# Kernel tuning notes

Measured on AMD Instinct MI355X. Metric: run time of the kernel, lower is better.

The kernel has to match this reference:

```python
import jax, jax.numpy as jnp
import numpy as np

K = 4
V = 32000
H = 512
B = 16
SOS = 1
EOS = 2


def setup_inputs() -> dict:
    key = jax.random.key(0)
    ks = jax.random.split(key, 8)
    s = 0.08  # small init keeps GRU/log_softmax well-conditioned
    return {
        "enc_h": jax.random.normal(ks[0], (B, H), jnp.float32),
        "E": jax.random.normal(ks[1], (V, H), jnp.float32) * s,
        "W_ih": jax.random.normal(ks[2], (H, 3 * H), jnp.float32) * s,
        "W_hh": jax.random.normal(ks[3], (H, 3 * H), jnp.float32) * s,
        "b_ih": jax.random.normal(ks[4], (3 * H,), jnp.float32) * s,
        "b_hh": jax.random.normal(ks[5], (3 * H,), jnp.float32) * s,
        "Wo": jax.random.normal(ks[6], (H, V), jnp.float32) * s,
        "bo": jax.random.normal(ks[7], (V,), jnp.float32) * s,
        "max_length": 32,
    }


def _beam_search(enc_h, E, W_ih, W_hh, b_ih, b_hh, Wo, bo, T):
    BK = B * K
    pos = jnp.arange(B, dtype=jnp.int32) * K  # pos_index
    # torch .repeat beam inflation: tiled layout (index i -> original i % B)
    h0 = jnp.tile(enc_h, (K, 1))  # [BK, H]
    inp0 = jnp.full((BK,), SOS, dtype=jnp.int32)
    ss0 = jnp.full((BK,), -jnp.inf, dtype=enc_h.dtype).at[pos].set(0.0)

    def gru(x, h):
        gi = x @ W_ih + b_ih
        gh = h @ W_hh + b_hh
        ir, iz, inn = jnp.split(gi, 3, axis=-1)
        hr, hz, hn = jnp.split(gh, 3, axis=-1)
        r = jax.nn.sigmoid(ir + hr)
        z = jax.nn.sigmoid(iz + hz)
        n = jnp.tanh(inn + r * hn)
        return (1.0 - z) * n + z * h

    def fwd_step(carry, _):
        inp, h, ss = carry
        h_new = gru(E[inp], h)                                   # [BK, H]
        logp = jax.nn.log_softmax(h_new @ Wo + bo, axis=-1)      # [BK, V]
        total = (ss[:, None] + logp).reshape(B, K * V)
        scores, cand = jax.lax.top_k(total, K)                   # [B, K]
        symbols = (cand % V).astype(jnp.int32).reshape(-1)       # input_var
        preds = (cand // V + pos[:, None]).astype(jnp.int32).reshape(-1)
        h_sel = h_new[preds]                                     # index_select hidden
        ss_new = scores.reshape(-1)
        ss_masked = jnp.where(symbols == EOS, -jnp.inf, ss_new)  # EOS masking
        return (symbols, h_sel, ss_masked), (logp, ss_new, preds, symbols, h_sel)

    _, (logps, step_scores, preds, syms, hiddens) = jax.lax.scan(
        fwd_step, (inp0, h0, ss0), None, length=T)

    # ---------------- backtrack ----------------
    last = step_scores[-1].reshape(B, K)
    s0, sorted_idx = jax.lax.top_k(last, K)
    tpred0 = (sorted_idx.astype(jnp.int32) + pos[:, None]).reshape(-1)
    lens0 = jnp.full((B, K), T, dtype=jnp.int32)
    hn0 = jnp.zeros((BK, H), dtype=enc_h.dtype)
    eos0 = jnp.zeros((B,), dtype=jnp.int32)

    def bt_step(carry, xs):
        tpred, eosf, s, lens, hn = carry
        logp_t, hid_t, pred_t, sym_t, score_t, tt = xs
        cur_out = logp_t[tpred]
        cur_hid = hid_t[tpred]
        cur_sym = sym_t[tpred]
        new_pred = pred_t[tpred]
        eos = sym_t == EOS
        eos_bk = eos.reshape(B, K).astype(jnp.int32)
        # original loop processes eos hits in descending beam order per batch
        higher = jnp.cumsum(eos_bk[:, ::-1], axis=1)[:, ::-1] - eos_bk
        occ = eosf[:, None] + higher
        res_k = K - occ % K - 1
        res_flat = (pos[:, None] + res_k).reshape(-1)
        idx = jnp.where(eos, res_flat, BK)  # BK = out of bounds -> dropped
        new_pred = new_pred.at[idx].set(pred_t, mode='drop')
        cur_out = cur_out.at[idx].set(logp_t, mode='drop')
        cur_hid = cur_hid.at[idx].set(hid_t, mode='drop')
        hn = hn.at[idx].set(hid_t, mode='drop')
        cur_sym = cur_sym.at[idx].set(sym_t, mode='drop')
        s = s.reshape(-1).at[idx].set(score_t, mode='drop').reshape(B, K)
        lens = lens.reshape(-1).at[idx].set(tt + 1, mode='drop').reshape(B, K)
        eosf = eosf + eos_bk.sum(axis=1)
        return (new_pred, eosf, s, lens, hn), (cur_out, cur_sym)

    ts = jnp.arange(T - 1, -1, -1, dtype=jnp.int32)
    (_, _, s_fin, lens_fin, hn_fin), (outs_rev, syms_rev) = jax.lax.scan(
        bt_step, (tpred0, eos0, s0, lens0, hn0),
        (logps[::-1], hiddens[::-1], preds[::-1], syms[::-1], step_scores[::-1], ts))

    s_sorted, re_idx = jax.lax.top_k(s_fin, K)
    lens_sorted = jnp.take_along_axis(lens_fin, re_idx, axis=1)
    re_flat = (re_idx.astype(jnp.int32) + pos[:, None]).reshape(-1)
    outs = outs_rev[::-1][:, re_flat].reshape(T, B, K, V)
    seqs = syms_rev[::-1][:, re_flat].reshape(T, B, K)
    decoder_outputs = outs[:, :, 0, :]            # [T, B, V]
    decoder_hidden = hn_fin[re_flat].reshape(B, K, H)[:, 0, :]
    return decoder_outputs, decoder_hidden, s_sorted, lens_sorted, seqs


def reference(enc_h, E, W_ih, W_hh, b_ih, b_hh, Wo, bo, max_length):
    return _beam_search(enc_h, E, W_ih, W_hh, b_ih, b_hh, Wo, bo, int(max_length))
```

## Files before the change

kernel.cpp:

```cpp
#include <hip/hip_runtime.h>
#include <math.h>
#include <limits.h>

#define T_STEPS 32
#define BATCH   16
#define KBEAM   4
#define BKR     64
#define HD      512
#define VOC     32000
#define G3      1536
#define SOS_TOK 1
#define EOS_TOK 2
#define NSP     (VOC/64)
#define NE      (NSP*4)

#define OFF_HCUR   ((size_t)0)
#define OFF_GBUF   (OFF_HCUR + (size_t)BKR*HD)
#define OFF_HNEW   (OFF_GBUF + (size_t)2*BKR*G3)
#define OFF_LSE    (OFF_HNEW + (size_t)T_STEPS*BKR*HD)
#define OFF_SS     (OFF_LSE + (size_t)T_STEPS*BKR)
#define OFF_SCORES (OFF_SS + BKR)
#define OFF_HNFIN  (OFF_SCORES + (size_t)T_STEPS*BKR)
#define OFF_PV     (OFF_HNFIN + (size_t)BKR*HD)
#define OFF_PM     (OFF_PV + (size_t)BKR*NE)
#define OFF_PS     (OFF_PM + (size_t)BKR*NSP)
#define OFF_FEND   (OFF_PS + (size_t)BKR*NSP)
#define IOFF_INP    0
#define IOFF_PREDS  64
#define IOFF_SYMS   (IOFF_PREDS + T_STEPS*BKR)
#define IOFF_RMAP   (IOFF_SYMS + T_STEPS*BKR)
#define IOFF_PC     (IOFF_RMAP + T_STEPS*BATCH)
#define IOFF_END    (IOFF_PC + BKR*NE)

#define O_HID  ((size_t)T_STEPS*BATCH*VOC)
#define O_SSRT (O_HID + (size_t)BATCH*HD)
#define O_LENS (O_SSRT + BATCH*KBEAM)
#define O_SEQS (O_LENS + BATCH*KBEAM)

typedef short bf16x8 __attribute__((ext_vector_type(8)));
typedef float f32x4  __attribute__((ext_vector_type(4)));

__device__ __forceinline__ unsigned short f2bf(float x){
    unsigned u = __float_as_uint(x);
    return (unsigned short)((u + 0x7fffu + ((u >> 16) & 1u)) >> 16);
}
__device__ __forceinline__ float bf2f(unsigned short h){
    return __uint_as_float(((unsigned)h) << 16);
}

__device__ __forceinline__ void mfma_core(
    const float* __restrict__ Abase, const int* __restrict__ ridx, int mbase,
    const float* __restrict__ B, int ldb, int n0,
    unsigned short (&Ah)[64][40], unsigned short (&Al)[64][40],
    unsigned short (&Bh)[64][40], unsigned short (&Bl)[64][40],
    int (&sidx)[64], f32x4 (&acc)[4])
{
    const int tid = threadIdx.x;
    if (tid < 64) sidx[tid] = ridx ? ridx[mbase + tid] : (mbase + tid);
    #pragma unroll
    for (int g = 0; g < 4; ++g) acc[g] = (f32x4){0.f, 0.f, 0.f, 0.f};
    const int wave = tid >> 6, lane = tid & 63;
    const int am = tid >> 2, ak0 = (tid & 3) * 8;
    const int bn = tid & 63, br0 = (tid >> 6) * 8;
    __syncthreads();
    const float* bcol = B + n0 + bn;
    for (int kt = 0; kt < 16; ++kt){
        {
            const float* ap = Abase + (size_t)sidx[am] * HD + kt * 32 + ak0;
            float4 x0 = *(const float4*)ap, x1 = *(const float4*)(ap + 4);
            float xs[8] = {x0.x, x0.y, x0.z, x0.w, x1.x, x1.y, x1.z, x1.w};
            union { unsigned short u[8]; uint4 v; } h8, l8;
            #pragma unroll
            for (int j = 0; j < 8; ++j){
                unsigned short h = f2bf(xs[j]);
                h8.u[j] = h; l8.u[j] = f2bf(xs[j] - bf2f(h));
            }
            *(uint4*)&Ah[am][ak0] = h8.v;
            *(uint4*)&Al[am][ak0] = l8.v;
        }
        {
            const float* bp = bcol + (size_t)(kt * 32 + br0) * ldb;
            union { unsigned short u[8]; uint4 v; } h8, l8;
            #pragma unroll
            for (int j = 0; j < 8; ++j){
                float x = bp[(size_t)j * ldb];
                unsigned short h = f2bf(x);
                h8.u[j] = h; l8.u[j] = f2bf(x - bf2f(h));
            }
            *(uint4*)&Bh[bn][br0] = h8.v;
            *(uint4*)&Bl[bn][br0] = l8.v;
        }
        __syncthreads();
        bf16x8 bh = *(const bf16x8*)&Bh[wave * 16 + (lane & 15)][(lane >> 4) * 8];
        bf16x8 bl = *(const bf16x8*)&Bl[wave * 16 + (lane & 15)][(lane >> 4) * 8];
        #pragma unroll
        for (int g = 0; g < 4; ++g){
            bf16x8 ah = *(const bf16x8*)&Ah[g * 16 + (lane & 15)][(lane >> 4) * 8];
            bf16x8 al = *(const bf16x8*)&Al[g * 16 + (lane & 15)][(lane >> 4) * 8];
            acc[g] = __builtin_amdgcn_mfma_f32_16x16x32_bf16(ah, bh, acc[g], 0, 0, 0);
            acc[g] = __builtin_amdgcn_mfma_f32_16x16x32_bf16(ah, bl, acc[g], 0, 0, 0);
            acc[g] = __builtin_amdgcn_mfma_f32_16x16x32_bf16(al, bh, acc[g], 0, 0, 0);
        }
        __syncthreads();
    }
}

__device__ __forceinline__ void dump_C(f32x4 (&acc)[4], float (&Cs)[64][65], int wave, int lane){
    #pragma unroll
    for (int g = 0; g < 4; ++g){
        int row = g * 16 + (lane >> 4) * 4;
        int col = wave * 16 + (lane & 15);
        #pragma unroll
        for (int r = 0; r < 4; ++r) Cs[row + r][col] = acc[g][r];
    }
}

__global__ __launch_bounds__(256) void gates_mfma_kernel(
    const float* __restrict__ E, const int* __restrict__ inp, const float* __restrict__ h_cur,
    const float* __restrict__ W_ih, const float* __restrict__ W_hh,
    const float* __restrict__ b_ih, const float* __restrict__ b_hh,
    float* __restrict__ gbuf)
{
    __shared__ unsigned short Ah[64][40], Al[64][40], Bh[64][40], Bl[64][40];
    __shared__ int sidx[64];
    __shared__ float Cs[64][65];
    const int z = blockIdx.y;
    const int n0 = blockIdx.x * 64;
    const int tid = threadIdx.x;
    f32x4 acc[4];
    mfma_core(z ? h_cur : E, z ? nullptr : inp, 0,
              z ? W_hh : W_ih, G3, n0, Ah, Al, Bh, Bl, sidx, acc);
    dump_C(acc, Cs, tid >> 6, tid & 63);
    __syncthreads();
    const float* bias = z ? b_hh : b_ih;
    const int row = tid >> 2, c0 = (tid & 3) * 16;
    float* gp = gbuf + (size_t)z * BKR * G3 + (size_t)row * G3 + n0 + c0;
    #pragma unroll
    for (int q = 0; q < 4; ++q){
        float4 bz = *(const float4*)(bias + n0 + c0 + q * 4);
        float4 v;
        v.x = Cs[row][c0 + q*4 + 0] + bz.x;
        v.y = Cs[row][c0 + q*4 + 1] + bz.y;
        v.z = Cs[row][c0 + q*4 + 2] + bz.z;
        v.w = Cs[row][c0 + q*4 + 3] + bz.w;
        *(float4*)(gp + q * 4) = v;
    }
}

__global__ void gru_combine_kernel(const float* __restrict__ gbuf, const float* __restrict__ h_cur,
    float* __restrict__ h_new)
{
    int x = blockIdx.x * 256 + threadIdx.x;
    int i = x >> 9, j = x & 511;
    const float* gi = gbuf + (size_t)i * G3;
    const float* gh = gbuf + (size_t)BKR * G3 + (size_t)i * G3;
    float ir = gi[j], iz = gi[j + 512], inn = gi[j + 1024];
    float hr = gh[j], hz = gh[j + 512], hnv = gh[j + 1024];
    float r  = 1.f / (1.f + expf(-(ir + hr)));
    float zz = 1.f / (1.f + expf(-(iz + hz)));
    float n  = tanhf(inn + r * hnv);
    h_new[x] = (1.f - zz) * n + zz * h_cur[x];
}

__device__ __forceinline__ void ins4(float* bv, int* bc, float s, int c){
    bool g0 = (s > bv[0]) || (s == bv[0] && c < bc[0]);
    bool g1 = (s > bv[1]) || (s == bv[1] && c < bc[1]);
    bool g2 = (s > bv[2]) || (s == bv[2] && c < bc[2]);
    bool g3 = (s > bv[3]) || (s == bv[3] && c < bc[3]);
    if (g0){ bv[3]=bv[2];bc[3]=bc[2]; bv[2]=bv[1];bc[2]=bc[1]; bv[1]=bv[0];bc[1]=bc[0]; bv[0]=s; bc[0]=c; }
    else if (g1){ bv[3]=bv[2];bc[3]=bc[2]; bv[2]=bv[1];bc[2]=bc[1]; bv[1]=s; bc[1]=c; }
    else if (g2){ bv[3]=bv[2];bc[3]=bc[2]; bv[2]=s; bc[2]=c; }
    else if (g3){ bv[3]=s; bc[3]=c; }
}

__global__ __launch_bounds__(256) void logits_topk_kernel(const float* __restrict__ h_new,
    const float* __restrict__ Wo, const float* __restrict__ bo,
    float* __restrict__ pv, int* __restrict__ pc, float* __restrict__ pm, float* __restrict__ ps)
{
    __shared__ unsigned short Ah[64][40], Al[64][40], Bh[64][40], Bl[64][40];
    __shared__ int sidx[64];
    __shared__ float Cs[64][65];
    const int bx = blockIdx.x, n0 = bx * 64;
    const int tid = threadIdx.x;
    f32x4 acc[4];
    mfma_core(h_new, nullptr, 0, Wo, VOC, n0, Ah, Al, Bh, Bl, sidx, acc);
    dump_C(acc, Cs, tid >> 6, tid & 63);
    __syncthreads();
    const int row = tid >> 2, c0 = (tid & 3) * 16;
    float bv[4] = {-INFINITY,-INFINITY,-INFINITY,-INFINITY};
    int bc[4] = {INT_MAX, INT_MAX, INT_MAX, INT_MAX};
    float m = -INFINITY, s = 0.f;
    #pragma unroll
    for (int j = 0; j < 16; ++j){
        float x = Cs[row][c0 + j] + bo[n0 + c0 + j];
        if (x > m){ s = s * expf(m - x) + 1.f; m = x; }
        else s += expf(x - m);
        ins4(bv, bc, x, n0 + c0 + j);
    }
    #pragma unroll
    for (int o = 1; o < 4; o <<= 1){
        float ov[4]; int oc[4];
        #pragma unroll
        for (int q = 0; q < 4; ++q){ ov[q] = __shfl_xor(bv[q], o); oc[q] = __shfl_xor(bc[q], o); }
        #pragma unroll
        for (int q = 0; q < 4; ++q) ins4(bv, bc, ov[q], oc[q]);
        float m2 = __shfl_xor(m, o), s2 = __shfl_xor(s, o);
        float M = fmaxf(m, m2);
        s = s * expf(m - M) + s2 * expf(m2 - M);
        m = M;
    }
    if ((tid & 3) == 0){
        const size_t base = (size_t)row * NE + (size_t)bx * 4;
        #pragma unroll
        for (int q = 0; q < 4; ++q){ pv[base + q] = bv[q]; pc[base + q] = bc[q]; }
        pm[row * NSP + bx] = m; ps[row * NSP + bx] = s;
    }
}

__global__ __launch_bounds__(256) void final_mfma_kernel(const float* __restrict__ h_new_all,
    const int* __restrict__ rmap, const float* __restrict__ lse_all,
    const float* __restrict__ Wo, const float* __restrict__ bo, float* __restrict__ out)
{
    __shared__ unsigned short Ah[64][40], Al[64][40], Bh[64][40], Bl[64][40];
    __shared__ int sidx[64];
    __shared__ float Cs[64][65];
    __shared__ float subm[64];
    const int n0 = blockIdx.x * 64, mb = blockIdx.y * 64;
    const int tid = threadIdx.x;
    f32x4 acc[4];
    mfma_core(h_new_all, rmap, mb, Wo, VOC, n0, Ah, Al, Bh, Bl, sidx, acc);
    dump_C(acc, Cs, tid >> 6, tid & 63);
    if (tid < 64) subm[tid] = lse_all[sidx[tid]];
    __syncthreads();
    const int row = tid >> 2, c0 = (tid & 3) * 16;
    const float sub = subm[row];
    float* op = out + (size_t)(mb + row) * VOC + n0 + c0;
    #pragma unroll
    for (int q = 0; q < 4; ++q){
        float4 bz = *(const float4*)(bo + n0 + c0 + q * 4);
        float4 v;
        v.x = Cs[row][c0 + q*4 + 0] + bz.x - sub;
        v.y = Cs[row][c0 + q*4 + 1] + bz.y - sub;
        v.z = Cs[row][c0 + q*4 + 2] + bz.z - sub;
        v.w = Cs[row][c0 + q*4 + 3] + bz.w - sub;
        *(float4*)(op + q * 4) = v;
    }
}

__global__ __launch_bounds__(256) void topk_phase_b(
    const float* __restrict__ pv, const int* __restrict__ pc,
    const float* __restrict__ pm, const float* __restrict__ ps,
    int t,
    float* __restrict__ scores_all, int* __restrict__ preds_all, int* __restrict__ syms_all,
    float* __restrict__ ss, int* __restrict__ inp, float* __restrict__ lse_all,
    const float* __restrict__ h_new, float* __restrict__ h_cur)
{
    const int b = blockIdx.x, tid = threadIdx.x;
    const int wave = tid >> 6, lane = tid & 63;
    const int row = b * KBEAM + wave;

    float bv[4] = {-INFINITY,-INFINITY,-INFINITY,-INFINITY};
    int bc[4] = {INT_MAX, INT_MAX, INT_MAX, INT_MAX};
    for (int e = lane; e < NE; e += 64)
        ins4(bv, bc, pv[(size_t)row * NE + e], pc[(size_t)row * NE + e]);
    #pragma unroll
    for (int o = 1; o < 64; o <<= 1){
        float ov[4]; int oc[4];
        #pragma unroll
        for (int q = 0; q < 4; ++q){ ov[q] = __shfl_xor(bv[q], o); oc[q] = __shfl_xor(bc[q], o); }
        #pragma unroll
        for (int q = 0; q < 4; ++q) ins4(bv, bc, ov[q], oc[q]);
    }
    float m = -INFINITY, s = 0.f;
    for (int e = lane; e < NSP; e += 64){
        float m2 = pm[row * NSP + e], s2 = ps[row * NSP + e];
        float M = fmaxf(m, m2);
        s = s * expf(m - M) + s2 * expf(m2 - M);
        m = M;
    }
    #pragma unroll
    for (int o = 1; o < 64; o <<= 1){
        float m2 = __shfl_xor(m, o), s2 = __shfl_xor(s, o);
        float M = fmaxf(m, m2);
        s = s * expf(m - M) + s2 * expf(m2 - M);
        m = M;
    }
    __shared__ float rtv[KBEAM][4]; __shared__ int rtc[KBEAM][4];
    __shared__ float rlse[KBEAM];
    if (lane == 0){
        #pragma unroll
        for (int q = 0; q < 4; ++q){ rtv[wave][q] = bv[q]; rtc[wave][q] = bc[q]; }
        rlse[wave] = m + logf(s);
    }
    __syncthreads();
    __shared__ int spred[KBEAM];
    if (tid == 0){
        float gv[4] = {-INFINITY,-INFINITY,-INFINITY,-INFINITY};
        int gc[4] = {INT_MAX, INT_MAX, INT_MAX, INT_MAX};
        #pragma unroll
        for (int kl = 0; kl < KBEAM; ++kl){
            const int r2 = b * KBEAM + kl;
            float lse = rlse[kl];
            lse_all[t * BKR + r2] = lse;
            float off = ss[r2] - lse;
            if (off == -INFINITY){
                #pragma unroll
                for (int q = 0; q < 4; ++q) ins4(gv, gc, -INFINITY, kl * VOC + q);
            } else {
                #pragma unroll
                for (int q = 0; q < 4; ++q) ins4(gv, gc, rtv[kl][q] + off, kl * VOC + rtc[kl][q]);
            }
        }
        #pragma unroll
        for (int u = 0; u < KBEAM; ++u){
            int cand = gc[u]; float val = gv[u];
            int sym = cand % VOC; int pg = b * KBEAM + cand / VOC;
            int slot = b * KBEAM + u;
            scores_all[t * BKR + slot] = val;
            syms_all[t * BKR + slot] = sym;
            preds_all[t * BKR + slot] = pg;
            ss[slot] = (sym == EOS_TOK) ? -INFINITY : val;
            inp[slot] = sym;
            spred[u] = pg;
        }
    }
    __syncthreads();
    for (int x = tid; x < KBEAM * HD; x += 256){
        int u = x >> 9, j = x & 511;
        h_cur[(b * KBEAM + u) * HD + j] = h_new[spred[u] * HD + j];
    }
}

__global__ void init_kernel(const float* __restrict__ enc_h, float* __restrict__ h_cur,
    float* __restrict__ ss, int* __restrict__ inp)
{
    const int i = blockIdx.x;
    for (int j = threadIdx.x; j < HD; j += blockDim.x)
        h_cur[i * HD + j] = enc_h[(i & (BATCH - 1)) * HD + j];
    if (i == 0 && threadIdx.x < BKR){
        ss[threadIdx.x] = ((threadIdx.x & (KBEAM - 1)) == 0) ? 0.f : -INFINITY;
        inp[threadIdx.x] = SOS_TOK;
    }
}

__global__ __launch_bounds__(256) void backtrack_kernel(
    const float* __restrict__ scores_all, const int* __restrict__ preds_all, const int* __restrict__ syms_all,
    const float* __restrict__ h_new_all, float* __restrict__ hn_fin,
    int* __restrict__ rmap, float* __restrict__ out)
{
    __shared__ int   l_syms[T_STEPS*BKR];
    __shared__ int   l_preds[T_STEPS*BKR];
    __shared__ float l_scores[T_STEPS*BKR];
    __shared__ int   outrow_s[T_STEPS*BKR];
    __shared__ int   cursym_s[T_STEPS*BKR];
    __shared__ int tpred[64]; __shared__ float sfin[64]; __shared__ int lensq[64];
    __shared__ int eosf[BATCH];
    __shared__ int orow[64], csym[64], npred_s[64];
    __shared__ int cp_slot[64], cp_src[64]; __shared__ int nc_b[BATCH];
    __shared__ int reidx[64];
    const int tid = threadIdx.x;

    for (int x = tid; x < T_STEPS*BKR; x += 256){
        l_syms[x]   = syms_all[x];
        l_preds[x]  = preds_all[x];
        l_scores[x] = scores_all[x];
    }
    for (int x = tid; x < BKR*HD; x += 256) hn_fin[x] = 0.f;
    __syncthreads();

    if (tid < BATCH){
        const int b = tid;
        float v[KBEAM]; int used[KBEAM];
        #pragma unroll
        for (int k = 0; k < KBEAM; ++k){ v[k] = l_scores[(T_STEPS-1)*BKR + b*KBEAM + k]; used[k] = 0; }
        #pragma unroll
        for (int u = 0; u < KBEAM; ++u){
            int best = -1; float bvv = 0.f;
            #pragma unroll
            for (int k = 0; k < KBEAM; ++k) if (!used[k] && (best < 0 || v[k] > bvv)){ best = k; bvv = v[k]; }
            used[best] = 1;
            tpred[b*KBEAM+u] = b*KBEAM + best;
            sfin[b*KBEAM+u] = bvv;
            lensq[b*KBEAM+u] = T_STEPS;
        }
        eosf[b] = 0;
    }
    __syncthreads();

    for (int t = T_STEPS-1; t >= 0; --t){
        if (tid < 64){
            int tp = tpred[tid];
            orow[tid]    = tp;
            csym[tid]    = l_syms[t*BKR + tp];
            npred_s[tid] = l_preds[t*BKR + tp];
        }
        __syncthreads();
        if (tid < BATCH){
            const int b = tid;
            int eos[KBEAM]; int cnt = 0;
            #pragma unroll
            for (int k = 0; k < KBEAM; ++k) eos[k] = (l_syms[t*BKR + b*KBEAM + k] == EOS_TOK);
            int nc = 0;
            #pragma unroll
            for (int k = 0; k < KBEAM; ++k) if (eos[k]){
                int higher = 0;
                #pragma unroll
                for (int k2 = k+1; k2 < KBEAM; ++k2) higher += eos[k2];
                int occ = eosf[b] + higher;
                int rk = KBEAM - (occ % KBEAM) - 1;
                int slot = b*KBEAM + rk;
                int j = b*KBEAM + k;
                npred_s[slot] = l_preds[t*BKR + j];
                orow[slot]    = j;
                csym[slot]    = l_syms[t*BKR + j];
                sfin[slot]    = l_scores[t*BKR + j];
                lensq[slot]   = t + 1;
                cp_slot[b*KBEAM + nc] = slot;
                cp_src[b*KBEAM + nc]  = l_preds[t*BKR + j];
                ++nc; ++cnt;
            }
            nc_b[b] = nc;
            eosf[b] += cnt;
        }
        __syncthreads();
        if (tid < 64){
            outrow_s[t*BKR + tid] = orow[tid];
            cursym_s[t*BKR + tid] = csym[tid];
            tpred[tid] = npred_s[tid];
        }
        {
            const int e = tid >> 2;
            const int eb = e >> 2, eq = e & 3;
            if (eq < nc_b[eb]){
                const int slot = cp_slot[eb*KBEAM + eq];
                const int src  = cp_src[eb*KBEAM + eq];
                const float4* sp = (const float4*)(h_new_all + (size_t)(t*BKR + src)*HD);
                float4* dp = (float4*)(hn_fin + (size_t)slot*HD);
                for (int j = (tid & 3); j < HD/4; j += 4) dp[j] = sp[j];
            }
        }
        __syncthreads();
    }

    if (tid < BATCH){
        const int b = tid;
        float v[KBEAM]; int used[KBEAM];
        #pragma unroll
        for (int k = 0; k < KBEAM; ++k){ v[k] = sfin[b*KBEAM+k]; used[k] = 0; }
        #pragma unroll
        for (int u = 0; u < KBEAM; ++u){
            int best = -1; float bvv = 0.f;
            #pragma unroll
            for (int k = 0; k < KBEAM; ++k) if (!used[k] && (best < 0 || v[k] > bvv)){ best = k; bvv = v[k]; }
            used[best] = 1;
            reidx[b*KBEAM+u] = best;
            out[O_SSRT + b*KBEAM + u] = bvv;
            out[O_LENS + b*KBEAM + u] = (float)lensq[b*KBEAM + best];
        }
    }
    __syncthreads();
    for (int x = tid; x < T_STEPS*BATCH; x += 256){
        int t2 = x >> 4, b = x & 15;
        rmap[x] = t2*BKR + outrow_s[t2*BKR + b*KBEAM + reidx[b*KBEAM]];
    }
    for (int x = tid; x < T_STEPS*BKR; x += 256){
        int t2 = x >> 6, rem = x & 63, b = rem >> 2, k = rem & 3;
        out[O_SEQS + x] = (float)cursym_s[t2*BKR + b*KBEAM + reidx[b*KBEAM + k]];
    }
    for (int x = tid; x < BATCH*HD; x += 256){
        int b = x >> 9, j = x & 511;
        out[O_HID + x] = hn_fin[(b*KBEAM + reidx[b*KBEAM])*HD + j];
    }
}

extern "C" void kernel_launch(void* const* d_in, const int* in_sizes, int n_in,
                              void* d_out, int out_size, void* d_ws, size_t ws_size,
                              hipStream_t stream)
{
    const float* enc_h = (const float*)d_in[0];
    const float* E     = (const float*)d_in[1];
    const float* W_ih  = (const float*)d_in[2];
    const float* W_hh  = (const float*)d_in[3];
    const float* b_ih  = (const float*)d_in[4];
    const float* b_hh  = (const float*)d_in[5];
    const float* Wo    = (const float*)d_in[6];
    const float* bo    = (const float*)d_in[7];
    float* out = (float*)d_out;

    float* w = (float*)d_ws;
    float* h_cur      = w + OFF_HCUR;
    float* gbuf       = w + OFF_GBUF;
    float* h_new_all  = w + OFF_HNEW;
    float* lse_all    = w + OFF_LSE;
    float* ss         = w + OFF_SS;
    float* scores_all = w + OFF_SCORES;
    float* hn_fin     = w + OFF_HNFIN;
    float* pv         = w + OFF_PV;
    float* pm         = w + OFF_PM;
    float* ps         = w + OFF_PS;
    int* wi         = (int*)(w + OFF_FEND);
    int* inp        = wi + IOFF_INP;
    int* preds_all  = wi + IOFF_PREDS;
    int* syms_all   = wi + IOFF_SYMS;
    int* rmap       = wi + IOFF_RMAP;
    int* pc         = wi + IOFF_PC;

    init_kernel<<<dim3(BKR), 256, 0, stream>>>(enc_h, h_cur, ss, inp);
    for (int t = 0; t < T_STEPS; ++t){
        float* h_new_t = h_new_all + (size_t)t * BKR * HD;
        gates_mfma_kernel<<<dim3(G3/64, 2), 256, 0, stream>>>(E, inp, h_cur, W_ih, W_hh, b_ih, b_hh, gbuf);
        gru_combine_kernel<<<dim3(BKR*HD/256), 256, 0, stream>>>(gbuf, h_cur, h_new_t);
        logits_topk_kernel<<<dim3(NSP), 256, 0, stream>>>(h_new_t, Wo, bo, pv, pc, pm, ps);
        topk_phase_b<<<dim3(BATCH), 256, 0, stream>>>(pv, pc, pm, ps, t, scores_all, preds_all, syms_all,
                                                      ss, inp, lse_all, h_new_t, h_cur);
    }
    backtrack_kernel<<<dim3(1), 256, 0, stream>>>(scores_all, preds_all, syms_all, h_new_all, hn_fin,
                                                  rmap, out);
    final_mfma_kernel<<<dim3(NSP, T_STEPS*BATCH/64), 256, 0, stream>>>(h_new_all, rmap, lse_all, Wo, bo, out);
}
```

Baseline: 2.966 ms.

## Prepack weights and activations into split-bf16 tiles for MFMA GEMMs

Adds a prepack pass that converts Wo, W_ih and W_hh once per call into hi/lo bf16 pairs laid out in tile order. The GRU combine and top-k kernels now also emit hi/lo bf16 copies of the hidden state and the gathered embeddings. The per-step GEMMs and the final logits GEMM can then load pre-split operands with vector loads, instead of re-reading fp32 and converting inside every block. The final kernel also reuses each Wo tile across four row blocks. The new path depends on the workspace being large enough, adds extra memory for the packed copies, and runs the prepack on every call.

```diff
diff --git a/kernel.cpp b/kernel.cpp
--- a/kernel.cpp
+++ b/kernel.cpp
@@ -13,6 +13,8 @@
 #define EOS_TOK 2
 #define NSP     (VOC/64)
 #define NE      (NSP*4)
+#define NBG     (G3/64)
+#define FMBL    4
 
 #define OFF_HCUR   ((size_t)0)
 #define OFF_GBUF   (OFF_HCUR + (size_t)BKR*HD)
@@ -31,6 +33,17 @@
 #define IOFF_RMAP   (IOFF_SYMS + T_STEPS*BKR)
 #define IOFF_PC     (IOFF_RMAP + T_STEPS*BATCH)
 #define IOFF_END    (IOFF_PC + BKR*NE)
+#define S_WOH   ((size_t)0)
+#define S_WOL   (S_WOH + (size_t)NSP*16*2048)
+#define S_WGH   (S_WOL + (size_t)NSP*16*2048)
+#define S_WGL   (S_WGH + (size_t)2*NBG*16*2048)
+#define S_HNH   (S_WGL + (size_t)2*NBG*16*2048)
+#define S_HNL   (S_HNH + (size_t)T_STEPS*BKR*HD)
+#define S_HCH   (S_HNL + (size_t)T_STEPS*BKR*HD)
+#define S_HCL   (S_HCH + (size_t)BKR*HD)
+#define S_EIH   (S_HCL + (size_t)BKR*HD)
+#define S_EIL   (S_EIH + (size_t)BKR*HD)
+#define S_END   (S_EIL + (size_t)BKR*HD)
 
 #define O_HID  ((size_t)T_STEPS*BATCH*VOC)
 #define O_SSRT (O_HID + (size_t)BATCH*HD)
@@ -46,6 +59,223 @@
 }
 __device__ __forceinline__ float bf2f(unsigned short h){
     return __uint_as_float(((unsigned)h) << 16);
+}
+
+__device__ __forceinline__ void dump_C(f32x4 (&acc)[4], float (&Cs)[64][65], int wave, int lane){
+    #pragma unroll
+    for (int g = 0; g < 4; ++g){
+        int row = g * 16 + (lane >> 4) * 4;
+        int col = wave * 16 + (lane & 15);
+        #pragma unroll
+        for (int r = 0; r < 4; ++r) Cs[row + r][col] = acc[g][r];
+    }
+}
+
+__device__ __forceinline__ void ins4(float* bv, int* bc, float s, int c){
+    bool g0 = (s > bv[0]) || (s == bv[0] && c < bc[0]);
+    bool g1 = (s > bv[1]) || (s == bv[1] && c < bc[1]);
+    bool g2 = (s > bv[2]) || (s == bv[2] && c < bc[2]);
+    bool g3 = (s > bv[3]) || (s == bv[3] && c < bc[3]);
+    if (g0){ bv[3]=bv[2];bc[3]=bc[2]; bv[2]=bv[1];bc[2]=bc[1]; bv[1]=bv[0];bc[1]=bc[0]; bv[0]=s; bc[0]=c; }
+    else if (g1){ bv[3]=bv[2];bc[3]=bc[2]; bv[2]=bv[1];bc[2]=bc[1]; bv[1]=s; bc[1]=c; }
+    else if (g2){ bv[3]=bv[2];bc[3]=bc[2]; bv[2]=s; bc[2]=c; }
+    else if (g3){ bv[3]=s; bc[3]=c; }
+}
+
+
+__global__ __launch_bounds__(256) void prepack_kernel(const float* __restrict__ W, int N,
+    unsigned short* __restrict__ oh, unsigned short* __restrict__ ol)
+{
+    const int bx = blockIdx.x, kt = blockIdx.y, tid = threadIdx.x;
+    const int bn = tid >> 2, kq = (tid & 3) * 8;
+    union { unsigned short u[8]; uint4 v; } h8, l8;
+    #pragma unroll
+    for (int j = 0; j < 8; ++j){
+        float x = W[(size_t)(kt*32 + kq + j) * (size_t)N + bx*64 + bn];
+        unsigned short h = f2bf(x);
+        h8.u[j] = h; l8.u[j] = f2bf(x - bf2f(h));
+    }
+    const size_t base = ((size_t)bx*16 + kt) * 2048 + (size_t)tid * 8;
+    *(uint4*)(oh + base) = h8.v;
+    *(uint4*)(ol + base) = l8.v;
+}
+
+__device__ __forceinline__ void mfma_core_pre(
+    const unsigned short* __restrict__ ahg, const unsigned short* __restrict__ alg,
+    const unsigned short* __restrict__ bth, const unsigned short* __restrict__ btl,
+    unsigned short (&Ah)[64][40], unsigned short (&Al)[64][40],
+    unsigned short (&Bh)[64][40], unsigned short (&Bl)[64][40],
+    f32x4 (&acc)[4])
+{
+    const int tid = threadIdx.x;
+    const int row = tid >> 2, kq = (tid & 3) * 8;
+    const int wave = tid >> 6, lane = tid & 63;
+    #pragma unroll
+    for (int g = 0; g < 4; ++g) acc[g] = (f32x4){0.f, 0.f, 0.f, 0.f};
+    for (int kt = 0; kt < 16; ++kt){
+        *(uint4*)&Ah[row][kq] = *(const uint4*)(ahg + (size_t)row*512 + kt*32 + kq);
+        *(uint4*)&Al[row][kq] = *(const uint4*)(alg + (size_t)row*512 + kt*32 + kq);
+        *(uint4*)&Bh[row][kq] = *(const uint4*)(bth + (size_t)kt*2048 + (size_t)tid*8);
+        *(uint4*)&Bl[row][kq] = *(const uint4*)(btl + (size_t)kt*2048 + (size_t)tid*8);
+        __syncthreads();
+        bf16x8 bh = *(const bf16x8*)&Bh[wave*16 + (lane&15)][(lane>>4)*8];
+        bf16x8 bl = *(const bf16x8*)&Bl[wave*16 + (lane&15)][(lane>>4)*8];
+        #pragma unroll
+        for (int g = 0; g < 4; ++g){
+            bf16x8 ah = *(const bf16x8*)&Ah[g*16 + (lane&15)][(lane>>4)*8];
+            bf16x8 al = *(const bf16x8*)&Al[g*16 + (lane&15)][(lane>>4)*8];
+            acc[g] = __builtin_amdgcn_mfma_f32_16x16x32_bf16(ah, bh, acc[g], 0, 0, 0);
+            acc[g] = __builtin_amdgcn_mfma_f32_16x16x32_bf16(ah, bl, acc[g], 0, 0, 0);
+            acc[g] = __builtin_amdgcn_mfma_f32_16x16x32_bf16(al, bh, acc[g], 0, 0, 0);
+        }
+        __syncthreads();
+    }
+}
+
+__global__ __launch_bounds__(256) void gates_pre_kernel(
+    const unsigned short* __restrict__ eih, const unsigned short* __restrict__ eil,
+    const unsigned short* __restrict__ hch, const unsigned short* __restrict__ hcl,
+    const unsigned short* __restrict__ wgh, const unsigned short* __restrict__ wgl,
+    const float* __restrict__ b_ih, const float* __restrict__ b_hh,
+    float* __restrict__ gbuf)
+{
+    __shared__ unsigned short Ah[64][40], Al[64][40], Bh[64][40], Bl[64][40];
+    __shared__ float Cs[64][65];
+    const int z = blockIdx.y, bx = blockIdx.x, n0 = bx * 64;
+    const int tid = threadIdx.x;
+    const unsigned short* ahg = z ? hch : eih;
+    const unsigned short* alg = z ? hcl : eil;
+    const size_t bt = ((size_t)z*NBG + bx) * 16 * 2048;
+    f32x4 acc[4];
+    mfma_core_pre(ahg, alg, wgh + bt, wgl + bt, Ah, Al, Bh, Bl, acc);
+    dump_C(acc, Cs, tid >> 6, tid & 63);
+    __syncthreads();
+    const float* bias = z ? b_hh : b_ih;
+    const int row = tid >> 2, c0 = (tid & 3) * 16;
+    float* gp = gbuf + (size_t)z * BKR * G3 + (size_t)row * G3 + n0 + c0;
+    #pragma unroll
+    for (int q = 0; q < 4; ++q){
+        float4 bz = *(const float4*)(bias + n0 + c0 + q * 4);
+        float4 v;
+        v.x = Cs[row][c0 + q*4 + 0] + bz.x;
+        v.y = Cs[row][c0 + q*4 + 1] + bz.y;
+        v.z = Cs[row][c0 + q*4 + 2] + bz.z;
+        v.w = Cs[row][c0 + q*4 + 3] + bz.w;
+        *(float4*)(gp + q * 4) = v;
+    }
+}
+
+__global__ __launch_bounds__(256) void logits_pre_kernel(
+    const unsigned short* __restrict__ hnh, const unsigned short* __restrict__ hnl,
+    const unsigned short* __restrict__ woh, const unsigned short* __restrict__ wol,
+    const float* __restrict__ bo,
+    float* __restrict__ pv, int* __restrict__ pc, float* __restrict__ pm, float* __restrict__ ps)
+{
+    __shared__ unsigned short Ah[64][40], Al[64][40], Bh[64][40], Bl[64][40];
+    __shared__ float Cs[64][65];
+    const int bx = blockIdx.x, n0 = bx * 64;
+    const int tid = threadIdx.x;
+    const size_t bt = (size_t)bx * 16 * 2048;
+    f32x4 acc[4];
+    mfma_core_pre(hnh, hnl, woh + bt, wol + bt, Ah, Al, Bh, Bl, acc);
+    dump_C(acc, Cs, tid >> 6, tid & 63);
+    __syncthreads();
+    const int row = tid >> 2, c0 = (tid & 3) * 16;
+    float bv[4] = {-INFINITY,-INFINITY,-INFINITY,-INFINITY};
+    int bc[4] = {INT_MAX, INT_MAX, INT_MAX, INT_MAX};
+    float m = -INFINITY, s = 0.f;
+    #pragma unroll
+    for (int j = 0; j < 16; ++j){
+        float x = Cs[row][c0 + j] + bo[n0 + c0 + j];
+        if (x > m){ s = s * expf(m - x) + 1.f; m = x; }
+        else s += expf(x - m);
+        ins4(bv, bc, x, n0 + c0 + j);
+    }
+    #pragma unroll
+    for (int o = 1; o < 4; o <<= 1){
+        float ov[4]; int oc[4];
+        #pragma unroll
+        for (int q = 0; q < 4; ++q){ ov[q] = __shfl_xor(bv[q], o); oc[q] = __shfl_xor(bc[q], o); }
+        #pragma unroll
+        for (int q = 0; q < 4; ++q) ins4(bv, bc, ov[q], oc[q]);
+        float m2 = __shfl_xor(m, o), s2 = __shfl_xor(s, o);
+        float M = fmaxf(m, m2);
+        s = s * expf(m - M) + s2 * expf(m2 - M);
+        m = M;
+    }
+    if ((tid & 3) == 0){
+        const size_t base = (size_t)row * NE + (size_t)bx * 4;
+        #pragma unroll
+        for (int q = 0; q < 4; ++q){ pv[base + q] = bv[q]; pc[base + q] = bc[q]; }
+        pm[row * NSP + bx] = m; ps[row * NSP + bx] = s;
+    }
+}
+
+__global__ __launch_bounds__(256) void final_pre_kernel(
+    const unsigned short* __restrict__ hnh, const unsigned short* __restrict__ hnl,
+    const int* __restrict__ rmap, const float* __restrict__ lse_all,
+    const unsigned short* __restrict__ woh, const unsigned short* __restrict__ wol,
+    const float* __restrict__ bo, float* __restrict__ out)
+{
+    __shared__ unsigned short Ah[64][40], Al[64][40], Bh[64][40], Bl[64][40];
+    __shared__ float Cs[64][65];
+    __shared__ int sidx[256]; __shared__ float subm[256];
+    const int tid = threadIdx.x;
+    const int bx = blockIdx.x, n0 = bx * 64;
+    const int mbase = blockIdx.y * (64 * FMBL);
+    sidx[tid] = rmap[mbase + tid];
+    __syncthreads();
+    subm[tid] = lse_all[sidx[tid]];
+    f32x4 acc[FMBL][4];
+    #pragma unroll
+    for (int mb = 0; mb < FMBL; ++mb)
+        #pragma unroll
+        for (int g = 0; g < 4; ++g) acc[mb][g] = (f32x4){0.f, 0.f, 0.f, 0.f};
+    const unsigned short* bth = woh + (size_t)bx * 16 * 2048;
+    const unsigned short* btl = wol + (size_t)bx * 16 * 2048;
+    const int row = tid >> 2, kq = (tid & 3) * 8;
+    const int wave = tid >> 6, lane = tid & 63;
+    for (int kt = 0; kt < 16; ++kt){
+        *(uint4*)&Bh[row][kq] = *(const uint4*)(bth + (size_t)kt*2048 + (size_t)tid*8);
+        *(uint4*)&Bl[row][kq] = *(const uint4*)(btl + (size_t)kt*2048 + (size_t)tid*8);
+        #pragma unroll
+        for (int mb = 0; mb < FMBL; ++mb){
+            const int g = sidx[mb*64 + row];
+            *(uint4*)&Ah[row][kq] = *(const uint4*)(hnh + (size_t)g*512 + kt*32 + kq);
+            *(uint4*)&Al[row][kq] = *(const uint4*)(hnl + (size_t)g*512 + kt*32 + kq);
+            __syncthreads();
+            bf16x8 bh = *(const bf16x8*)&Bh[wave*16 + (lane&15)][(lane>>4)*8];
+            bf16x8 bl = *(const bf16x8*)&Bl[wave*16 + (lane&15)][(lane>>4)*8];
+            #pragma unroll
+            for (int gg = 0; gg < 4; ++gg){
+                bf16x8 ah = *(const bf16x8*)&Ah[gg*16 + (lane&15)][(lane>>4)*8];
+                bf16x8 al = *(const bf16x8*)&Al[gg*16 + (lane&15)][(lane>>4)*8];
+                acc[mb][gg] = __builtin_amdgcn_mfma_f32_16x16x32_bf16(ah, bh, acc[mb][gg], 0, 0, 0);
+                acc[mb][gg] = __builtin_amdgcn_mfma_f32_16x16x32_bf16(ah, bl, acc[mb][gg], 0, 0, 0);
+                acc[mb][gg] = __builtin_amdgcn_mfma_f32_16x16x32_bf16(al, bh, acc[mb][gg], 0, 0, 0);
+            }
+            __syncthreads();
+        }
+    }
+    const int r = tid >> 2, c0 = (tid & 3) * 16;
+    #pragma unroll
+    for (int mb = 0; mb < FMBL; ++mb){
+        dump_C(acc[mb], Cs, wave, lane);
+        __syncthreads();
+        const float sub = subm[mb*64 + r];
+        float* op = out + (size_t)(mbase + mb*64 + r) * VOC + n0 + c0;
+        #pragma unroll
+        for (int q = 0; q < 4; ++q){
+            float4 bz = *(const float4*)(bo + n0 + c0 + q * 4);
+            float4 v;
+            v.x = Cs[r][c0 + q*4 + 0] + bz.x - sub;
+            v.y = Cs[r][c0 + q*4 + 1] + bz.y - sub;
+            v.z = Cs[r][c0 + q*4 + 2] + bz.z - sub;
+            v.w = Cs[r][c0 + q*4 + 3] + bz.w - sub;
+            *(float4*)(op + q * 4) = v;
+        }
+        __syncthreads();
+    }
 }
 
 __device__ __forceinline__ void mfma_core(
@@ -105,16 +335,6 @@
     }
 }
 
-__device__ __forceinline__ void dump_C(f32x4 (&acc)[4], float (&Cs)[64][65], int wave, int lane){
-    #pragma unroll
-    for (int g = 0; g < 4; ++g){
-        int row = g * 16 + (lane >> 4) * 4;
-        int col = wave * 16 + (lane & 15);
-        #pragma unroll
-        for (int r = 0; r < 4; ++r) Cs[row + r][col] = acc[g][r];
-    }
-}
-
 __global__ __launch_bounds__(256) void gates_mfma_kernel(
     const float* __restrict__ E, const int* __restrict__ inp, const float* __restrict__ h_cur,
     const float* __restrict__ W_ih, const float* __restrict__ W_hh,
@@ -147,8 +367,83 @@
     }
 }
 
+__global__ __launch_bounds__(256) void logits_topk_kernel(const float* __restrict__ h_new,
+    const float* __restrict__ Wo, const float* __restrict__ bo,
+    float* __restrict__ pv, int* __restrict__ pc, float* __restrict__ pm, float* __restrict__ ps)
+{
+    __shared__ unsigned short Ah[64][40], Al[64][40], Bh[64][40], Bl[64][40];
+    __shared__ int sidx[64];
+    __shared__ float Cs[64][65];
+    const int bx = blockIdx.x, n0 = bx * 64;
+    const int tid = threadIdx.x;
+    f32x4 acc[4];
+    mfma_core(h_new, nullptr, 0, Wo, VOC, n0, Ah, Al, Bh, Bl, sidx, acc);
+    dump_C(acc, Cs, tid >> 6, tid & 63);
+    __syncthreads();
+    const int row = tid >> 2, c0 = (tid & 3) * 16;
+    float bv[4] = {-INFINITY,-INFINITY,-INFINITY,-INFINITY};
+    int bc[4] = {INT_MAX, INT_MAX, INT_MAX, INT_MAX};
+    float m = -INFINITY, s = 0.f;
+    #pragma unroll
+    for (int j = 0; j < 16; ++j){
+        float x = Cs[row][c0 + j] + bo[n0 + c0 + j];
+        if (x > m){ s = s * expf(m - x) + 1.f; m = x; }
+        else s += expf(x - m);
+        ins4(bv, bc, x, n0 + c0 + j);
+    }
+    #pragma unroll
+    for (int o = 1; o < 4; o <<= 1){
+        float ov[4]; int oc[4];
+        #pragma unroll
+        for (int q = 0; q < 4; ++q){ ov[q] = __shfl_xor(bv[q], o); oc[q] = __shfl_xor(bc[q], o); }
+        #pragma unroll
+        for (int q = 0; q < 4; ++q) ins4(bv, bc, ov[q], oc[q]);
+        float m2 = __shfl_xor(m, o), s2 = __shfl_xor(s, o);
+        float M = fmaxf(m, m2);
+        s = s * expf(m - M) + s2 * expf(m2 - M);
+        m = M;
+    }
+    if ((tid & 3) == 0){
+        const size_t base = (size_t)row * NE + (size_t)bx * 4;
+        #pragma unroll
+        for (int q = 0; q < 4; ++q){ pv[base + q] = bv[q]; pc[base + q] = bc[q]; }
+        pm[row * NSP + bx] = m; ps[row * NSP + bx] = s;
+    }
+}
+
+__global__ __launch_bounds__(256) void final_mfma_kernel(const float* __restrict__ h_new_all,
+    const int* __restrict__ rmap, const float* __restrict__ lse_all,
+    const float* __restrict__ Wo, const float* __restrict__ bo, float* __restrict__ out)
+{
+    __shared__ unsigned short Ah[64][40], Al[64][40], Bh[64][40], Bl[64][40];
+    __shared__ int sidx[64];
+    __shared__ float Cs[64][65];
+    __shared__ float subm[64];
+    const int n0 = blockIdx.x * 64, mb = blockIdx.y * 64;
+    const int tid = threadIdx.x;
+    f32x4 acc[4];
+    mfma_core(h_new_all, rmap, mb, Wo, VOC, n0, Ah, Al, Bh, Bl, sidx, acc);
+    dump_C(acc, Cs, tid >> 6, tid & 63);
+    if (tid < 64) subm[tid] = lse_all[sidx[tid]];
+    __syncthreads();
+    const int row = tid >> 2, c0 = (tid & 3) * 16;
+    const float sub = subm[row];
+    float* op = out + (size_t)(mb + row) * VOC + n0 + c0;
+    #pragma unroll
+    for (int q = 0; q < 4; ++q){
+        float4 bz = *(const float4*)(bo + n0 + c0 + q * 4);
+        float4 v;
+        v.x = Cs[row][c0 + q*4 + 0] + bz.x - sub;
+        v.y = Cs[row][c0 + q*4 + 1] + bz.y - sub;
+        v.z = Cs[row][c0 + q*4 + 2] + bz.z - sub;
+        v.w = Cs[row][c0 + q*4 + 3] + bz.w - sub;
+        *(float4*)(op + q * 4) = v;
+    }
+}
+
+
 __global__ void gru_combine_kernel(const float* __restrict__ gbuf, const float* __restrict__ h_cur,
-    float* __restrict__ h_new)
+    float* __restrict__ h_new, unsigned short* __restrict__ hnh, unsigned short* __restrict__ hnl)
 {
     int x = blockIdx.x * 256 + threadIdx.x;
     int i = x >> 9, j = x & 511;
@@ -159,91 +454,11 @@
     float r  = 1.f / (1.f + expf(-(ir + hr)));
     float zz = 1.f / (1.f + expf(-(iz + hz)));
     float n  = tanhf(inn + r * hnv);
-    h_new[x] = (1.f - zz) * n + zz * h_cur[x];
-}
-
-__device__ __forceinline__ void ins4(float* bv, int* bc, float s, int c){
-    bool g0 = (s > bv[0]) || (s == bv[0] && c < bc[0]);
-    bool g1 = (s > bv[1]) || (s == bv[1] && c < bc[1]);
-    bool g2 = (s > bv[2]) || (s == bv[2] && c < bc[2]);
-    bool g3 = (s > bv[3]) || (s == bv[3] && c < bc[3]);
-    if (g0){ bv[3]=bv[2];bc[3]=bc[2]; bv[2]=bv[1];bc[2]=bc[1]; bv[1]=bv[0];bc[1]=bc[0]; bv[0]=s; bc[0]=c; }
-    else if (g1){ bv[3]=bv[2];bc[3]=bc[2]; bv[2]=bv[1];bc[2]=bc[1]; bv[1]=s; bc[1]=c; }
-    else if (g2){ bv[3]=bv[2];bc[3]=bc[2]; bv[2]=s; bc[2]=c; }
-    else if (g3){ bv[3]=s; bc[3]=c; }
-}
-
-__global__ __launch_bounds__(256) void logits_topk_kernel(const float* __restrict__ h_new,
-    const float* __restrict__ Wo, const float* __restrict__ bo,
-    float* __restrict__ pv, int* __restrict__ pc, float* __restrict__ pm, float* __restrict__ ps)
-{
-    __shared__ unsigned short Ah[64][40], Al[64][40], Bh[64][40], Bl[64][40];
-    __shared__ int sidx[64];
-    __shared__ float Cs[64][65];
-    const int bx = blockIdx.x, n0 = bx * 64;
-    const int tid = threadIdx.x;
-    f32x4 acc[4];
-    mfma_core(h_new, nullptr, 0, Wo, VOC, n0, Ah, Al, Bh, Bl, sidx, acc);
-    dump_C(acc, Cs, tid >> 6, tid & 63);
-    __syncthreads();
-    const int row = tid >> 2, c0 = (tid & 3) * 16;
-    float bv[4] = {-INFINITY,-INFINITY,-INFINITY,-INFINITY};
-    int bc[4] = {INT_MAX, INT_MAX, INT_MAX, INT_MAX};
-    float m = -INFINITY, s = 0.f;
-    #pragma unroll
-    for (int j = 0; j < 16; ++j){
-        float x = Cs[row][c0 + j] + bo[n0 + c0 + j];
-        if (x > m){ s = s * expf(m - x) + 1.f; m = x; }
-        else s += expf(x - m);
-        ins4(bv, bc, x, n0 + c0 + j);
-    }
-    #pragma unroll
-    for (int o = 1; o < 4; o <<= 1){
-        float ov[4]; int oc[4];
-        #pragma unroll
-        for (int q = 0; q < 4; ++q){ ov[q] = __shfl_xor(bv[q], o); oc[q] = __shfl_xor(bc[q], o); }
-        #pragma unroll
-        for (int q = 0; q < 4; ++q) ins4(bv, bc, ov[q], oc[q]);
-        float m2 = __shfl_xor(m, o), s2 = __shfl_xor(s, o);
-        float M = fmaxf(m, m2);
-        s = s * expf(m - M) + s2 * expf(m2 - M);
-        m = M;
-    }
-    if ((tid & 3) == 0){
-        const size_t base = (size_t)row * NE + (size_t)bx * 4;
-        #pragma unroll
-        for (int q = 0; q < 4; ++q){ pv[base + q] = bv[q]; pc[base + q] = bc[q]; }
-        pm[row * NSP + bx] = m; ps[row * NSP + bx] = s;
-    }
-}
-
-__global__ __launch_bounds__(256) void final_mfma_kernel(const float* __restrict__ h_new_all,
-    const int* __restrict__ rmap, const float* __restrict__ lse_all,
-    const float* __restrict__ Wo, const float* __restrict__ bo, float* __restrict__ out)
-{
-    __shared__ unsigned short Ah[64][40], Al[64][40], Bh[64][40], Bl[64][40];
-    __shared__ int sidx[64];
-    __shared__ float Cs[64][65];
-    __shared__ float subm[64];
-    const int n0 = blockIdx.x * 64, mb = blockIdx.y * 64;
-    const int tid = threadIdx.x;
-    f32x4 acc[4];
-    mfma_core(h_new_all, rmap, mb, Wo, VOC, n0, Ah, Al, Bh, Bl, sidx, acc);
-    dump_C(acc, Cs, tid >> 6, tid & 63);
-    if (tid < 64) subm[tid] = lse_all[sidx[tid]];
-    __syncthreads();
-    const int row = tid >> 2, c0 = (tid & 3) * 16;
-    const float sub = subm[row];
-    float* op = out + (size_t)(mb + row) * VOC + n0 + c0;
-    #pragma unroll
-    for (int q = 0; q < 4; ++q){
-        float4 bz = *(const float4*)(bo + n0 + c0 + q * 4);
-        float4 v;
-        v.x = Cs[row][c0 + q*4 + 0] + bz.x - sub;
-        v.y = Cs[row][c0 + q*4 + 1] + bz.y - sub;
-        v.z = Cs[row][c0 + q*4 + 2] + bz.z - sub;
-        v.w = Cs[row][c0 + q*4 + 3] + bz.w - sub;
-        *(float4*)(op + q * 4) = v;
+    float v = (1.f - zz) * n + zz * h_cur[x];
+    h_new[x] = v;
+    if (hnh){
+        unsigned short h = f2bf(v);
+        hnh[x] = h; hnl[x] = f2bf(v - bf2f(h));
     }
 }
 
@@ -253,7 +468,10 @@
     int t,
     float* __restrict__ scores_all, int* __restrict__ preds_all, int* __restrict__ syms_all,
     float* __restrict__ ss, int* __restrict__ inp, float* __restrict__ lse_all,
-    const float* __restrict__ h_new, float* __restrict__ h_cur)
+    const float* __restrict__ h_new, float* __restrict__ h_cur,
+    const float* __restrict__ E,
+    unsigned short* __restrict__ hch, unsigned short* __restrict__ hcl,
+    unsigned short* __restrict__ eih, unsigned short* __restrict__ eil)
 {
     const int b = blockIdx.x, tid = threadIdx.x;
     const int wave = tid >> 6, lane = tid & 63;
@@ -293,7 +511,7 @@
         rlse[wave] = m + logf(s);
     }
     __syncthreads();
-    __shared__ int spred[KBEAM];
+    __shared__ int spred[KBEAM]; __shared__ int ssym[KBEAM];
     if (tid == 0){
         float gv[4] = {-INFINITY,-INFINITY,-INFINITY,-INFINITY};
         int gc[4] = {INT_MAX, INT_MAX, INT_MAX, INT_MAX};
@@ -321,22 +539,43 @@
             preds_all[t * BKR + slot] = pg;
             ss[slot] = (sym == EOS_TOK) ? -INFINITY : val;
             inp[slot] = sym;
-            spred[u] = pg;
+            spred[u] = pg; ssym[u] = sym;
         }
     }
     __syncthreads();
     for (int x = tid; x < KBEAM * HD; x += 256){
         int u = x >> 9, j = x & 511;
-        h_cur[(b * KBEAM + u) * HD + j] = h_new[spred[u] * HD + j];
-    }
-}
-
-__global__ void init_kernel(const float* __restrict__ enc_h, float* __restrict__ h_cur,
-    float* __restrict__ ss, int* __restrict__ inp)
+        const int idx = (b * KBEAM + u) * HD + j;
+        float v = h_new[spred[u] * HD + j];
+        h_cur[idx] = v;
+        if (hch){
+            unsigned short h = f2bf(v);
+            hch[idx] = h; hcl[idx] = f2bf(v - bf2f(h));
+            float e = E[(size_t)ssym[u] * HD + j];
+            unsigned short eh = f2bf(e);
+            eih[idx] = eh; eil[idx] = f2bf(e - bf2f(eh));
+        }
+    }
+}
+
+__global__ void init_kernel(const float* __restrict__ enc_h, const float* __restrict__ E,
+    float* __restrict__ h_cur, float* __restrict__ ss, int* __restrict__ inp,
+    unsigned short* __restrict__ hch, unsigned short* __restrict__ hcl,
+    unsigned short* __restrict__ eih, unsigned short* __restrict__ eil)
 {
     const int i = blockIdx.x;
-    for (int j = threadIdx.x; j < HD; j += blockDim.x)
-        h_cur[i * HD + j] = enc_h[(i & (BATCH - 1)) * HD + j];
+    for (int j = threadIdx.x; j < HD; j += blockDim.x){
+        float v = enc_h[(i & (BATCH - 1)) * HD + j];
+        h_cur[i * HD + j] = v;
+        if (hch){
+            const int idx = i * HD + j;
+            unsigned short h = f2bf(v);
+            hch[idx] = h; hcl[idx] = f2bf(v - bf2f(h));
+            float e = E[(size_t)SOS_TOK * HD + j];
+            unsigned short eh = f2bf(e);
+            eih[idx] = eh; eil[idx] = f2bf(e - bf2f(eh));
+        }
+    }
     if (i == 0 && threadIdx.x < BKR){
         ss[threadIdx.x] = ((threadIdx.x & (KBEAM - 1)) == 0) ? 0.f : -INFINITY;
         inp[threadIdx.x] = SOS_TOK;
@@ -504,17 +743,56 @@
     int* syms_all   = wi + IOFF_SYMS;
     int* rmap       = wi + IOFF_RMAP;
     int* pc         = wi + IOFF_PC;
-
-    init_kernel<<<dim3(BKR), 256, 0, stream>>>(enc_h, h_cur, ss, inp);
+    unsigned short* sb = (unsigned short*)(wi + IOFF_END);
+    unsigned short* woh = sb + S_WOH;
+    unsigned short* wol = sb + S_WOL;
+    unsigned short* wgh = sb + S_WGH;
+    unsigned short* wgl = sb + S_WGL;
+    unsigned short* hnh = sb + S_HNH;
+    unsigned short* hnl = sb + S_HNL;
+    unsigned short* hch = sb + S_HCH;
+    unsigned short* hcl = sb + S_HCL;
+    unsigned short* eih = sb + S_EIH;
+    unsigned short* eil = sb + S_EIL;
+
+    const size_t NEED = (size_t)OFF_FEND*4 + (size_t)IOFF_END*4 + (size_t)S_END*2;
+    const bool pre = (ws_size >= NEED);
+
+    init_kernel<<<dim3(BKR), 256, 0, stream>>>(enc_h, E, h_cur, ss, inp,
+        pre ? hch : nullptr, hcl, eih, eil);
+    if (pre){
+        prepack_kernel<<<dim3(NSP, 16), 256, 0, stream>>>(Wo, VOC, woh, wol);
+        prepack_kernel<<<dim3(NBG, 16), 256, 0, stream>>>(W_ih, G3, wgh, wgl);
+        prepack_kernel<<<dim3(NBG, 16), 256, 0, stream>>>(W_hh, G3,
+            wgh + (size_t)NBG*16*2048, wgl + (size_t)NBG*16*2048);
+    }
     for (int t = 0; t < T_STEPS; ++t){
         float* h_new_t = h_new_all + (size_t)t * BKR * HD;
-        gates_mfma_kernel<<<dim3(G3/64, 2), 256, 0, stream>>>(E, inp, h_cur, W_ih, W_hh, b_ih, b_hh, gbuf);
-        gru_combine_kernel<<<dim3(BKR*HD/256), 256, 0, stream>>>(gbuf, h_cur, h_new_t);
-        logits_topk_kernel<<<dim3(NSP), 256, 0, stream>>>(h_new_t, Wo, bo, pv, pc, pm, ps);
+        unsigned short* hnh_t = hnh + (size_t)t * BKR * HD;
+        unsigned short* hnl_t = hnl + (size_t)t * BKR * HD;
+        if (pre){
+            gates_pre_kernel<<<dim3(NBG, 2), 256, 0, stream>>>(eih, eil, hch, hcl,
+                wgh, wgl, b_ih, b_hh, gbuf);
+        } else {
+            gates_mfma_kernel<<<dim3(NBG, 2), 256, 0, stream>>>(E, inp, h_cur, W_ih, W_hh, b_ih, b_hh, gbuf);
+        }
+        gru_combine_kernel<<<dim3(BKR*HD/256), 256, 0, stream>>>(gbuf, h_cur, h_new_t,
+            pre ? hnh_t : nullptr, hnl_t);
+        if (pre){
+            logits_pre_kernel<<<dim3(NSP), 256, 0, stream>>>(hnh_t, hnl_t, woh, wol, bo, pv, pc, pm, ps);
+        } else {
+            logits_topk_kernel<<<dim3(NSP), 256, 0, stream>>>(h_new_t, Wo, bo, pv, pc, pm, ps);
+        }
         topk_phase_b<<<dim3(BATCH), 256, 0, stream>>>(pv, pc, pm, ps, t, scores_all, preds_all, syms_all,
-                                                      ss, inp, lse_all, h_new_t, h_cur);
+            ss, inp, lse_all, h_new_t, h_cur, E,
+            pre ? hch : nullptr, hcl, eih, eil);
     }
     backtrack_kernel<<<dim3(1), 256, 0, stream>>>(scores_all, preds_all, syms_all, h_new_all, hn_fin,
                                                   rmap, out);
-    final_mfma_kernel<<<dim3(NSP, T_STEPS*BATCH/64), 256, 0, stream>>>(h_new_all, rmap, lse_all, Wo, bo, out);
-}
+    if (pre){
+        final_pre_kernel<<<dim3(NSP, (T_STEPS*BATCH)/(64*FMBL)), 256, 0, stream>>>(
+            hnh, hnl, rmap, lse_all, woh, wol, bo, out);
+    } else {
+        final_mfma_kernel<<<dim3(NSP, T_STEPS*BATCH/64), 256, 0, stream>>>(h_new_all, rmap, lse_all, Wo, bo, out);
+    }
+}
```

Measured after the change: 2.787 ms. 6.0% less time.
